# Performance work log

Hardware: AMD Instinct MI355X
Metric: run time of the kernel (lower is better)

The kernel has to match this reference:

```python
import jax, jax.numpy as jnp
import numpy as np

NUM_BLOCKS = 8
BLOCK_SIZE = 96
HIDDEN_FACTOR = 1
B, H, W = 1, 360, 181


def setup_inputs() -> dict:
    key = jax.random.key(0)
    k_inp, k_w, k_b = jax.random.split(key, 3)
    out_size = BLOCK_SIZE * HIDDEN_FACTOR
    inp = jax.random.normal(k_inp, (B, NUM_BLOCKS, BLOCK_SIZE, H, W, 2), dtype=jnp.float32)
    weight = jax.random.normal(k_w, (NUM_BLOCKS, BLOCK_SIZE, out_size, 2), dtype=jnp.float32) * 0.02
    bias = jax.random.normal(k_b, (NUM_BLOCKS, out_size, 1, 1, 2), dtype=jnp.float32) * 0.02
    return {"inp": inp, "weight": weight, "bias": bias}


def reference(inp, weight, bias):
    # inp:    [b, k, i, x, y, 2]  (last dim = real/imag)
    # weight: [k, i, o, 2]; bias: [k, o, 1, 1, 2]
    ar, ai = inp[..., 0], inp[..., 1]
    wr, wi = weight[..., 0], weight[..., 1]
    # complex matmul: (ar + i*ai) @ (wr + i*wi), block-diagonal over k
    real = jnp.einsum("bkixy,kio->bkoxy", ar, wr) - jnp.einsum("bkixy,kio->bkoxy", ai, wi)
    imag = jnp.einsum("bkixy,kio->bkoxy", ai, wr) + jnp.einsum("bkixy,kio->bkoxy", ar, wi)
    return jnp.stack([real, imag], axis=-1) + bias  # [b, k, o, x, y, 2]
```

## Files before the change

### kernel.cpp

```cpp
#include <hip/hip_runtime.h>

#define XY 65160
#define NI 96
#define NO 96
#define NK 8
#define NT2 510

typedef __attribute__((ext_vector_type(8))) short short8;
typedef __attribute__((ext_vector_type(4))) float floatx4;

union FragU { short8 v; unsigned u[4]; };

static __device__ __forceinline__ unsigned cvt_pk(float lo, float hi) {
    unsigned r;
    asm("v_cvt_pk_bf16_f32 %0, %1, %2" : "=v"(r) : "v"(lo), "v"(hi));
    return r;
}

__global__ __launch_bounds__(512, 4) void cmult_kernel(
    const float* __restrict__ inp, const float* __restrict__ weight,
    const float* __restrict__ bias, float* __restrict__ out)
{
    __shared__ unsigned wlds[36 * 64 * 4];
    __shared__ float2 blds[NO];

    const int tid  = threadIdx.x;
    const int lane = tid & 63;
    const int wave = tid >> 6;
    const int h    = wave & 1;
    const int g    = wave >> 1;
    const int k    = blockIdx.y;
    const int l15  = lane & 15;
    const int quad = lane >> 4;

    const float* wk   = weight + (size_t)k * NI * NO * 2;
    const float* inpk = inp    + (size_t)k * NI * XY * 2;

    for (int idx = tid; idx < NI * NO; idx += 512) {
        int i = idx / NO;
        int o = idx - i * NO;
        float2 w = *reinterpret_cast<const float2*>(wk + (size_t)idx * 2);
        int s = i >> 4, q = (i >> 2) & 3, t = i & 3;
        int m = o >> 4, c = o & 15;
        wlds[((s * 6 + m) * 64 + (q * 16 + c)) * 4 + t] = cvt_pk(w.x, w.y);
    }
    if (tid < NO) {
        blds[tid] = *reinterpret_cast<const float2*>(bias + ((size_t)k * NO + tid) * 2);
    }
    __syncthreads();

    for (int tidx = blockIdx.x; tidx < NT2; tidx += gridDim.x) {
        int x0  = tidx * 128 + g * 32 + 2 * l15;
        int x0c = x0 <= XY - 2 ? x0 : XY - 2;

        floatx4 accRA[3], accIA[3], accRB[3], accIB[3];
        #pragma unroll
        for (int m = 0; m < 3; ++m) {
            accRA[m] = (floatx4){0.f,0.f,0.f,0.f}; accIA[m] = (floatx4){0.f,0.f,0.f,0.f};
            accRB[m] = (floatx4){0.f,0.f,0.f,0.f}; accIB[m] = (floatx4){0.f,0.f,0.f,0.f};
        }

        #pragma unroll
        for (int s = 0; s < 6; ++s) {
            FragU bNA, bSA, bNB, bSB;
            #pragma unroll
            for (int t = 0; t < 4; ++t) {
                int i = 16 * s + 4 * quad + t;
                float4 a = *reinterpret_cast<const float4*>(inpk + ((size_t)i * XY + x0c) * 2);
                unsigned pA = cvt_pk(a.x, a.y);
                unsigned pB = cvt_pk(a.z, a.w);
                bNA.u[t] = pA ^ 0x80000000u;
                bSA.u[t] = (pA >> 16) | (pA << 16);
                bNB.u[t] = pB ^ 0x80000000u;
                bSB.u[t] = (pB >> 16) | (pB << 16);
            }
            #pragma unroll
            for (int mm = 0; mm < 3; ++mm) {
                int m = 3 * h + mm;
                FragU wf;
                uint4 wp = *(reinterpret_cast<const uint4*>(wlds) + (s * 6 + m) * 64 + lane);
                wf.u[0] = wp.x; wf.u[1] = wp.y; wf.u[2] = wp.z; wf.u[3] = wp.w;
                accRA[mm] = __builtin_amdgcn_mfma_f32_16x16x32_bf16(wf.v, bNA.v, accRA[mm], 0, 0, 0);
                accIA[mm] = __builtin_amdgcn_mfma_f32_16x16x32_bf16(wf.v, bSA.v, accIA[mm], 0, 0, 0);
                accRB[mm] = __builtin_amdgcn_mfma_f32_16x16x32_bf16(wf.v, bNB.v, accRB[mm], 0, 0, 0);
                accIB[mm] = __builtin_amdgcn_mfma_f32_16x16x32_bf16(wf.v, bSB.v, accIB[mm], 0, 0, 0);
            }
        }

        if (x0 < XY) {
            #pragma unroll
            for (int mm = 0; mm < 3; ++mm) {
                #pragma unroll
                for (int r = 0; r < 4; ++r) {
                    int o = 16 * (3 * h + mm) + 4 * quad + r;
                    float2 b = blds[o];
                    float4 ov;
                    ov.x = accRA[mm][r] + b.x;
                    ov.y = accIA[mm][r] + b.y;
                    ov.z = accRB[mm][r] + b.x;
                    ov.w = accIB[mm][r] + b.y;
                    *reinterpret_cast<float4*>(out + ((size_t)(k * NO + o) * XY + x0) * 2) = ov;
                }
            }
        }
    }
}

extern "C" void kernel_launch(void* const* d_in, const int* in_sizes, int n_in,
                              void* d_out, int out_size, void* d_ws, size_t ws_size,
                              hipStream_t stream)
{
    const float* inp    = (const float*)d_in[0];
    const float* weight = (const float*)d_in[1];
    const float* bias   = (const float*)d_in[2];
    float* out = (float*)d_out;

    dim3 grid(128, NK), block(512);
    hipLaunchKernelGGL(cmult_kernel, grid, block, 0, stream, inp, weight, bias, out);
}
```

Before: 809.7 us.

## Give each wave all 96 outputs for 16 points instead of half outputs over 32

Each wave now covers 16 spatial points across all six output tiles, instead of 32 points (two per lane) across half the outputs. Inputs are read as float2 per lane rather than float4, so every input element is loaded and converted by one wave only, with no duplication across the wave pair. The cost is half as many points per memory instruction, narrower global loads and stores, and twice as many LDS weight-fragment reads per MFMA pair.

Result: no change. 796.9 us (-1.6%).

```diff
diff --git a/kernel.cpp b/kernel.cpp
--- a/kernel.cpp
+++ b/kernel.cpp
@@ -4,7 +4,7 @@
 #define NI 96
 #define NO 96
 #define NK 8
-#define NT2 510
+#define NT 510
 
 typedef __attribute__((ext_vector_type(8))) short short8;
 typedef __attribute__((ext_vector_type(4))) float floatx4;
@@ -27,8 +27,6 @@
     const int tid  = threadIdx.x;
     const int lane = tid & 63;
     const int wave = tid >> 6;
-    const int h    = wave & 1;
-    const int g    = wave >> 1;
     const int k    = blockIdx.y;
     const int l15  = lane & 15;
     const int quad = lane >> 4;
@@ -49,57 +47,49 @@
     }
     __syncthreads();
 
-    for (int tidx = blockIdx.x; tidx < NT2; tidx += gridDim.x) {
-        int x0  = tidx * 128 + g * 32 + 2 * l15;
-        int x0c = x0 <= XY - 2 ? x0 : XY - 2;
+    for (int tidx = blockIdx.x; tidx < NT; tidx += gridDim.x) {
+        int xy  = tidx * 128 + wave * 16 + l15;
+        int xyc = xy < XY ? xy : XY - 1;
 
-        floatx4 accRA[3], accIA[3], accRB[3], accIB[3];
+        floatx4 accR[6], accI[6];
         #pragma unroll
-        for (int m = 0; m < 3; ++m) {
-            accRA[m] = (floatx4){0.f,0.f,0.f,0.f}; accIA[m] = (floatx4){0.f,0.f,0.f,0.f};
-            accRB[m] = (floatx4){0.f,0.f,0.f,0.f}; accIB[m] = (floatx4){0.f,0.f,0.f,0.f};
+        for (int m = 0; m < 6; ++m) {
+            accR[m] = (floatx4){0.f,0.f,0.f,0.f};
+            accI[m] = (floatx4){0.f,0.f,0.f,0.f};
         }
 
         #pragma unroll
         for (int s = 0; s < 6; ++s) {
-            FragU bNA, bSA, bNB, bSB;
+            FragU bN, bS;
             #pragma unroll
             for (int t = 0; t < 4; ++t) {
                 int i = 16 * s + 4 * quad + t;
-                float4 a = *reinterpret_cast<const float4*>(inpk + ((size_t)i * XY + x0c) * 2);
-                unsigned pA = cvt_pk(a.x, a.y);
-                unsigned pB = cvt_pk(a.z, a.w);
-                bNA.u[t] = pA ^ 0x80000000u;
-                bSA.u[t] = (pA >> 16) | (pA << 16);
-                bNB.u[t] = pB ^ 0x80000000u;
-                bSB.u[t] = (pB >> 16) | (pB << 16);
+                float2 a = *reinterpret_cast<const float2*>(inpk + ((size_t)i * XY + xyc) * 2);
+                unsigned p = cvt_pk(a.x, a.y);
+                bN.u[t] = p ^ 0x80000000u;
+                bS.u[t] = (p >> 16) | (p << 16);
             }
             #pragma unroll
-            for (int mm = 0; mm < 3; ++mm) {
-                int m = 3 * h + mm;
+            for (int m = 0; m < 6; ++m) {
                 FragU wf;
                 uint4 wp = *(reinterpret_cast<const uint4*>(wlds) + (s * 6 + m) * 64 + lane);
                 wf.u[0] = wp.x; wf.u[1] = wp.y; wf.u[2] = wp.z; wf.u[3] = wp.w;
-                accRA[mm] = __builtin_amdgcn_mfma_f32_16x16x32_bf16(wf.v, bNA.v, accRA[mm], 0, 0, 0);
-                accIA[mm] = __builtin_amdgcn_mfma_f32_16x16x32_bf16(wf.v, bSA.v, accIA[mm], 0, 0, 0);
-                accRB[mm] = __builtin_amdgcn_mfma_f32_16x16x32_bf16(wf.v, bNB.v, accRB[mm], 0, 0, 0);
-                accIB[mm] = __builtin_amdgcn_mfma_f32_16x16x32_bf16(wf.v, bSB.v, accIB[mm], 0, 0, 0);
+                accR[m] = __builtin_amdgcn_mfma_f32_16x16x32_bf16(wf.v, bN.v, accR[m], 0, 0, 0);
+                accI[m] = __builtin_amdgcn_mfma_f32_16x16x32_bf16(wf.v, bS.v, accI[m], 0, 0, 0);
             }
         }
 
-        if (x0 < XY) {
+        if (xy < XY) {
             #pragma unroll
-            for (int mm = 0; mm < 3; ++mm) {
+            for (int m = 0; m < 6; ++m) {
                 #pragma unroll
                 for (int r = 0; r < 4; ++r) {
-                    int o = 16 * (3 * h + mm) + 4 * quad + r;
+                    int o = 16 * m + 4 * quad + r;
                     float2 b = blds[o];
-                    float4 ov;
-                    ov.x = accRA[mm][r] + b.x;
-                    ov.y = accIA[mm][r] + b.y;
-                    ov.z = accRB[mm][r] + b.x;
-                    ov.w = accIB[mm][r] + b.y;
-                    *reinterpret_cast<float4*>(out + ((size_t)(k * NO + o) * XY + x0) * 2) = ov;
+                    float2 ov;
+                    ov.x = accR[m][r] + b.x;
+                    ov.y = accI[m][r] + b.y;
+                    *reinterpret_cast<float2*>(out + ((size_t)(k * NO + o) * XY + xy) * 2) = ov;
                 }
             }
         }
```
